# Kernel optimization log

Hardware: AMD Instinct MI355X
Metric: run time of the kernel (lower is better)

## Reference

```python
import jax, jax.numpy as jnp
import numpy as np

IMAGE_SIZE = 128
PATCH_SIZE = 8
BOND_DIM = 128
CP_RANK = 64
EMBED_DIM = 512
BATCH = 512
GRID = IMAGE_SIZE // PATCH_SIZE            # 16
NUM_PATCHES = GRID * GRID                  # 256
DEPTH = 4                                  # log4(256)
LEVEL_NODES = [64, 16, 4, 1]


def setup_inputs() -> dict:
    key = jax.random.key(0)
    ks = jax.random.split(key, 32)
    s = 0.02
    inp = {
        "x": jax.random.normal(ks[0], (BATCH, 1, IMAGE_SIZE, IMAGE_SIZE), jnp.float32),
        "W_patch": jax.random.normal(ks[1], (PATCH_SIZE * PATCH_SIZE, BOND_DIM), jnp.float32) * s,
        "b_patch": jnp.zeros((BOND_DIM,), jnp.float32),
        "pos": jax.random.normal(ks[2], (1, NUM_PATCHES, BOND_DIM), jnp.float32),
        "gamma": jnp.ones((BOND_DIM,), jnp.float32),
        "beta": jnp.zeros((BOND_DIM,), jnp.float32),
        "W_head": jax.random.normal(ks[3], (BOND_DIM, EMBED_DIM), jnp.float32) * s,
        "b_head": jnp.zeros((EMBED_DIM,), jnp.float32),
    }
    for lvl, n in enumerate(LEVEL_NODES):
        # per-node distinct CP factors: 4 children in_dim->rank, then rank->out_dim
        inp[f"f{lvl}"] = jax.random.normal(ks[4 + 2 * lvl], (n, 4, BOND_DIM, CP_RANK), jnp.float32) * s
        inp[f"o{lvl}"] = jax.random.normal(ks[5 + 2 * lvl], (n, CP_RANK, BOND_DIM), jnp.float32) * s
    return inp


def _patchify(x):
    # 'b c (h p1) (w p2) -> b (h w) (p1 p2 c)', c == 1
    b = x.shape[0]
    x = x.reshape(b, 1, GRID, PATCH_SIZE, GRID, PATCH_SIZE)
    x = x.transpose(0, 2, 4, 3, 5, 1)                  # b h w p1 p2 c
    return x.reshape(b, NUM_PATCHES, PATCH_SIZE * PATCH_SIZE)


def _quad_group(x, grid):
    # 'b (h w) c -> b (h/2 w/2) (h2 w2) c' with 2x2 blocks
    b, _, c = x.shape
    g2 = grid // 2
    x = x.reshape(b, g2, 2, g2, 2, c).transpose(0, 1, 3, 2, 4, 5)
    return x.reshape(b, g2 * g2, 4, c)


def _cp_level(x, f, o):
    # x: [b, n, 4, C]; f: [n, 4, C, R]; o: [n, R, C]
    u = jnp.einsum('bnqc,nqcr->bnqr', x, f)
    p = jnp.prod(u, axis=2)                            # [b, n, R]
    return jnp.einsum('bnr,nrc->bnc', p, o)


def reference(x, W_patch, b_patch, pos, f0, o0, f1, o1, f2, o2, f3, o3,
              gamma, beta, W_head, b_head):
    h = _patchify(x) @ W_patch + b_patch               # [b, 256, C]
    h = h + pos
    grid = GRID
    for f, o in ((f0, o0), (f1, o1), (f2, o2), (f3, o3)):
        h = _cp_level(_quad_group(h, grid), f, o)
        grid //= 2
    h = h[:, 0, :]                                     # squeeze node dim
    mu = jnp.mean(h, axis=-1, keepdims=True)
    var = jnp.var(h, axis=-1, keepdims=True)
    h = (h - mu) / jnp.sqrt(var + 1e-5) * gamma + beta
    out = h @ W_head + b_head
    n = jnp.maximum(jnp.linalg.norm(out, axis=-1, keepdims=True), 1e-12)
    return out / n
```

## Files before the change

### kernel.cpp

```cpp
#include <hip/hip_runtime.h>
#include <hip/hip_bf16.h>

#define BATCH     512
#define IMG       128
#define PS        8
#define GRID_P    16
#define NP        256
#define C         128
#define R         64
#define E         512

typedef float f32x4 __attribute__((ext_vector_type(4)));
typedef short s16x8 __attribute__((ext_vector_type(8)));

__device__ __forceinline__ unsigned short f2bf(float x) {
    unsigned int u = __float_as_uint(x);
    u += 0x7fffu + ((u >> 16) & 1u);
    return (unsigned short)(u >> 16);
}
__device__ __forceinline__ float bf2f(unsigned short h) {
    return __uint_as_float(((unsigned int)h) << 16);
}

__global__ __launch_bounds__(256) void prep_kernel(
    const float* __restrict__ f0, const float* __restrict__ f1,
    const float* __restrict__ f2, const float* __restrict__ f3,
    const float* __restrict__ o0, const float* __restrict__ o1,
    const float* __restrict__ o2, const float* __restrict__ o3,
    const float* __restrict__ Wh, const float* __restrict__ Wp,
    unsigned short* __restrict__ fT, unsigned short* __restrict__ oT,
    unsigned short* __restrict__ WhT, unsigned short* __restrict__ Wp_bf)
{
    __shared__ float ls[128 * 68];
    const int bi = blockIdx.x, t = threadIdx.x;

    if (bi < 340) {
        const float* src;
        if      (bi < 256) src = f0 + (size_t)bi * 8192;
        else if (bi < 320) src = f1 + (size_t)(bi - 256) * 8192;
        else if (bi < 336) src = f2 + (size_t)(bi - 320) * 8192;
        else               src = f3 + (size_t)(bi - 336) * 8192;
        unsigned short* dst = fT + (size_t)bi * 8192;
#pragma unroll
        for (int i = 0; i < 8; ++i) {
            const int fi = (t + 256 * i) * 4;
            const int c = fi >> 6, r = fi & 63;
            *(float4*)(ls + c * 68 + r) = *(const float4*)(src + fi);
        }
        __syncthreads();
        const int rr = t >> 2, seg = t & 3;
        unsigned int* d32 = (unsigned int*)(dst + rr * 128 + seg * 32);
#pragma unroll
        for (int ii = 0; ii < 16; ++ii) {
            const int c = seg * 32 + ii * 2;
            const unsigned int lo = f2bf(ls[c * 68 + rr]);
            const unsigned int hi = f2bf(ls[(c + 1) * 68 + rr]);
            d32[ii] = lo | (hi << 16);
        }
    } else if (bi < 425) {
        const int oi = bi - 340;
        const float* src;
        if      (oi < 64) src = o0 + (size_t)oi * 8192;
        else if (oi < 80) src = o1 + (size_t)(oi - 64) * 8192;
        else if (oi < 84) src = o2 + (size_t)(oi - 80) * 8192;
        else              src = o3 + (size_t)(oi - 84) * 8192;
        unsigned short* dst = oT + (size_t)oi * 8192;
#pragma unroll
        for (int i = 0; i < 8; ++i) {
            const int fi = (t + 256 * i) * 4;
            const int r = fi >> 7, c = fi & 127;
            *(float4*)(ls + r * 132 + c) = *(const float4*)(src + fi);
        }
        __syncthreads();
        const int cc = t >> 1, seg = t & 1;
        unsigned int* d32 = (unsigned int*)(dst + cc * 64 + seg * 32);
#pragma unroll
        for (int ii = 0; ii < 16; ++ii) {
            const int r = seg * 32 + ii * 2;
            const unsigned int lo = f2bf(ls[r * 132 + cc]);
            const unsigned int hi = f2bf(ls[(r + 1) * 132 + cc]);
            d32[ii] = lo | (hi << 16);
        }
    } else if (bi < 433) {
        const int j = bi - 425;
#pragma unroll
        for (int i = 0; i < 8; ++i) {
            const int fi = (t + 256 * i) * 4;
            const int c = fi >> 6, e = fi & 63;
            *(float4*)(ls + c * 68 + e) = *(const float4*)(Wh + (size_t)c * E + j * 64 + e);
        }
        __syncthreads();
        const int rr = t >> 2, seg = t & 3;
        unsigned int* d32 = (unsigned int*)(WhT + (size_t)(j * 64 + rr) * 128 + seg * 32);
#pragma unroll
        for (int ii = 0; ii < 16; ++ii) {
            const int c = seg * 32 + ii * 2;
            const unsigned int lo = f2bf(ls[c * 68 + rr]);
            const unsigned int hi = f2bf(ls[(c + 1) * 68 + rr]);
            d32[ii] = lo | (hi << 16);
        }
    } else {
#pragma unroll
        for (int i = 0; i < 32; ++i) {
            const int idx = i * 256 + t;
            Wp_bf[idx] = f2bf(Wp[idx]);
        }
    }
}

__global__ __launch_bounds__(64) void wft_pf_kernel(
    const unsigned short* __restrict__ fT0,
    const unsigned short* __restrict__ Wp_bf,
    const float* __restrict__ pos, const float* __restrict__ bp,
    unsigned short* __restrict__ WfT,
    float* __restrict__ pf)
{
    const int bi = blockIdx.x;
    if (bi < 256) {
        const int blk  = bi;
        const int lane = threadIdx.x & 63;
        const int m = lane & 15, g = lane >> 4;
        const unsigned short* A = fT0 + (size_t)blk * 8192;

        f32x4 acc[4][4];
#pragma unroll
        for (int mt = 0; mt < 4; ++mt)
#pragma unroll
            for (int nt = 0; nt < 4; ++nt) acc[mt][nt] = (f32x4){0.f, 0.f, 0.f, 0.f};

#pragma unroll
        for (int kt = 0; kt < 4; ++kt) {
            const int koff = kt * 32 + g * 8;
            s16x8 afr[4], bfr[4];
#pragma unroll
            for (int mt = 0; mt < 4; ++mt)
                afr[mt] = *(const s16x8*)(A + (size_t)(mt * 16 + m) * 128 + koff);
#pragma unroll
            for (int nt = 0; nt < 4; ++nt)
                bfr[nt] = *(const s16x8*)(Wp_bf + (size_t)(nt * 16 + m) * 128 + koff);
#pragma unroll
            for (int mt = 0; mt < 4; ++mt)
#pragma unroll
                for (int nt = 0; nt < 4; ++nt)
                    acc[mt][nt] = __builtin_amdgcn_mfma_f32_16x16x32_bf16(afr[mt], bfr[nt], acc[mt][nt], 0, 0, 0);
        }

        unsigned short* D = WfT + (size_t)blk * 4096;
#pragma unroll
        for (int mt = 0; mt < 4; ++mt)
#pragma unroll
            for (int nt = 0; nt < 4; ++nt)
#pragma unroll
                for (int j = 0; j < 4; ++j)
                    D[(size_t)(mt * 16 + g * 4 + j) * 64 + nt * 16 + m] = f2bf(acc[mt][nt][j]);
    } else {
        const int blk = bi - 256;
        const int n = blk >> 2, q = blk & 3;
        const int r = threadIdx.x & 63;
        const int p = (2 * (n >> 3) + (q >> 1)) * GRID_P + 2 * (n & 7) + (q & 1);
        const unsigned short* frow = fT0 + (size_t)blk * 8192 + (size_t)r * 128;
        const float* pp = pos + (size_t)p * C;
        float s = 0.f;
#pragma unroll 4
        for (int c = 0; c < C; ++c) s += (pp[c] + bp[c]) * bf2f(frow[c]);
        pf[blk * 64 + r] = s;
    }
}

__global__ __launch_bounds__(256) void cp_level0_fused(
    const float* __restrict__ x,
    const unsigned short* __restrict__ WfT,
    const float* __restrict__ pf,
    const unsigned short* __restrict__ oT0,
    unsigned short* __restrict__ h1)
{
    constexpr int NN = 64;
    __shared__ __align__(16) float us[4 * 16 * 68];
    __shared__ __align__(16) unsigned short ps[16 * 72];

    const int bi = blockIdx.x;
    const int n = bi >> 5, btile = bi & 31;
    const int t = threadIdx.x, w = t >> 6, lane = t & 63;
    const int m = lane & 15, g = lane >> 4;
    const int bt = btile * 16;
    const int y1 = n >> 3, x1 = n & 7;
    const int b = bt + m;
    const int q = w;

    const int py = (2 * y1 + (q >> 1)) * PS;
    const int px = (2 * x1 + (q & 1)) * PS;
    s16x8 a[2];
#pragma unroll
    for (int kt = 0; kt < 2; ++kt) {
        const float* src = x + ((size_t)b * IMG + py + kt * 4 + g) * IMG + px;
        const float4 p0 = *(const float4*)src;
        const float4 p1 = *(const float4*)(src + 4);
        s16x8 v;
        v[0] = (short)f2bf(p0.x); v[1] = (short)f2bf(p0.y);
        v[2] = (short)f2bf(p0.z); v[3] = (short)f2bf(p0.w);
        v[4] = (short)f2bf(p1.x); v[5] = (short)f2bf(p1.y);
        v[6] = (short)f2bf(p1.z); v[7] = (short)f2bf(p1.w);
        a[kt] = v;
    }

    const float* pfq = pf + (size_t)(n * 4 + q) * 64;
    f32x4 acc_u[4];
#pragma unroll
    for (int nt = 0; nt < 4; ++nt) {
        const float pv = pfq[nt * 16 + m];
        acc_u[nt] = (f32x4){pv, pv, pv, pv};
    }
    const unsigned short* Wq = WfT + (size_t)(n * 4 + q) * 4096;
#pragma unroll
    for (int kt = 0; kt < 2; ++kt) {
        const int koff = kt * 32 + g * 8;
#pragma unroll
        for (int nt = 0; nt < 4; ++nt) {
            const s16x8 bfr = *(const s16x8*)(Wq + (size_t)(nt * 16 + m) * 64 + koff);
            acc_u[nt] = __builtin_amdgcn_mfma_f32_16x16x32_bf16(a[kt], bfr, acc_u[nt], 0, 0, 0);
        }
    }
#pragma unroll
    for (int nt = 0; nt < 4; ++nt)
#pragma unroll
        for (int j = 0; j < 4; ++j)
            us[(q * 16 + g * 4 + j) * 68 + nt * 16 + m] = acc_u[nt][j];
    __syncthreads();

    {
        const int pb = t >> 4, r0 = (t & 15) * 4;
        const f32x4 u0 = *(const f32x4*)(us + (0 * 16 + pb) * 68 + r0);
        const f32x4 u1 = *(const f32x4*)(us + (1 * 16 + pb) * 68 + r0);
        const f32x4 u2 = *(const f32x4*)(us + (2 * 16 + pb) * 68 + r0);
        const f32x4 u3 = *(const f32x4*)(us + (3 * 16 + pb) * 68 + r0);
        const f32x4 p = u0 * u1 * u2 * u3;
        uint2 v;
        v.x = (unsigned int)f2bf(p[0]) | ((unsigned int)f2bf(p[1]) << 16);
        v.y = (unsigned int)f2bf(p[2]) | ((unsigned int)f2bf(p[3]) << 16);
        *(uint2*)(ps + pb * 72 + r0) = v;
    }
    __syncthreads();

    const unsigned short* oTn = oT0 + (size_t)n * C * R;
    s16x8 ap[2];
#pragma unroll
    for (int kt = 0; kt < 2; ++kt)
        ap[kt] = *(const s16x8*)(ps + m * 72 + kt * 32 + g * 8);
    f32x4 aco[2];
#pragma unroll
    for (int i = 0; i < 2; ++i) {
        aco[i] = (f32x4){0.f, 0.f, 0.f, 0.f};
        const int ct = w * 2 + i;
#pragma unroll
        for (int kt = 0; kt < 2; ++kt) {
            const s16x8 bfr = *(const s16x8*)(oTn + (size_t)(ct * 16 + m) * R + kt * 32 + g * 8);
            aco[i] = __builtin_amdgcn_mfma_f32_16x16x32_bf16(ap[kt], bfr, aco[i], 0, 0, 0);
        }
    }
#pragma unroll
    for (int i = 0; i < 2; ++i)
#pragma unroll
        for (int j = 0; j < 4; ++j) {
            const int row = bt + g * 4 + j;
            h1[((size_t)row * NN + n) * C + (w * 2 + i) * 16 + m] = f2bf(aco[i][j]);
        }
}

template<int NN, int GIN>
__global__ __launch_bounds__(256) void cp_level_mfma4(
    const unsigned short* __restrict__ hin,
    const unsigned short* __restrict__ fT,
    const unsigned short* __restrict__ oT,
    unsigned short* __restrict__ hout)
{
    constexpr int NIN = GIN * GIN;
    constexpr int G2  = GIN / 2;
    __shared__ __align__(16) float us[4 * 16 * 68];
    __shared__ __align__(16) unsigned short ps[16 * 72];

    const int bi = blockIdx.x;
    const int n = bi >> 5, btile = bi & 31;
    const int t = threadIdx.x, w = t >> 6, lane = t & 63;
    const int m = lane & 15, g = lane >> 4;
    const int bt = btile * 16;
    const int y1 = n / G2, x1 = n % G2;
    const int q = w;

    const int pidx = (2 * y1 + (q >> 1)) * GIN + 2 * x1 + (q & 1);
    const unsigned short* xq = hin + ((size_t)(bt + m) * NIN + pidx) * C;
    const unsigned short* fq = fT + (size_t)(n * 4 + q) * R * C;

    f32x4 acc_u[4];
#pragma unroll
    for (int nt = 0; nt < 4; ++nt) acc_u[nt] = (f32x4){0.f, 0.f, 0.f, 0.f};
#pragma unroll
    for (int kt = 0; kt < 4; ++kt) {
        const int koff = kt * 32 + g * 8;
        const s16x8 a = *(const s16x8*)(xq + koff);
#pragma unroll
        for (int nt = 0; nt < 4; ++nt) {
            const s16x8 bfr = *(const s16x8*)(fq + (size_t)(nt * 16 + m) * C + koff);
            acc_u[nt] = __builtin_amdgcn_mfma_f32_16x16x32_bf16(a, bfr, acc_u[nt], 0, 0, 0);
        }
    }
#pragma unroll
    for (int nt = 0; nt < 4; ++nt)
#pragma unroll
        for (int j = 0; j < 4; ++j)
            us[(q * 16 + g * 4 + j) * 68 + nt * 16 + m] = acc_u[nt][j];
    __syncthreads();

    {
        const int pb = t >> 4, r0 = (t & 15) * 4;
        const f32x4 u0 = *(const f32x4*)(us + (0 * 16 + pb) * 68 + r0);
        const f32x4 u1 = *(const f32x4*)(us + (1 * 16 + pb) * 68 + r0);
        const f32x4 u2 = *(const f32x4*)(us + (2 * 16 + pb) * 68 + r0);
        const f32x4 u3 = *(const f32x4*)(us + (3 * 16 + pb) * 68 + r0);
        const f32x4 p = u0 * u1 * u2 * u3;
        uint2 v;
        v.x = (unsigned int)f2bf(p[0]) | ((unsigned int)f2bf(p[1]) << 16);
        v.y = (unsigned int)f2bf(p[2]) | ((unsigned int)f2bf(p[3]) << 16);
        *(uint2*)(ps + pb * 72 + r0) = v;
    }
    __syncthreads();

    const unsigned short* oTn = oT + (size_t)n * C * R;
    s16x8 ap[2];
#pragma unroll
    for (int kt = 0; kt < 2; ++kt)
        ap[kt] = *(const s16x8*)(ps + m * 72 + kt * 32 + g * 8);
    f32x4 aco[2];
#pragma unroll
    for (int i = 0; i < 2; ++i) {
        aco[i] = (f32x4){0.f, 0.f, 0.f, 0.f};
        const int ct = w * 2 + i;
#pragma unroll
        for (int kt = 0; kt < 2; ++kt) {
            const s16x8 bfr = *(const s16x8*)(oTn + (size_t)(ct * 16 + m) * R + kt * 32 + g * 8);
            aco[i] = __builtin_amdgcn_mfma_f32_16x16x32_bf16(ap[kt], bfr, aco[i], 0, 0, 0);
        }
    }
#pragma unroll
    for (int i = 0; i < 2; ++i)
#pragma unroll
        for (int j = 0; j < 4; ++j) {
            const int row = bt + g * 4 + j;
            hout[((size_t)row * NN + n) * C + (w * 2 + i) * 16 + m] = f2bf(aco[i][j]);
        }
}

__global__ __launch_bounds__(256) void tail_kernel(
    const unsigned short* __restrict__ h2,
    const unsigned short* __restrict__ fT2,
    const unsigned short* __restrict__ oT2,
    const unsigned short* __restrict__ fT3,
    const unsigned short* __restrict__ oT3,
    const float* __restrict__ gamma, const float* __restrict__ beta,
    const unsigned short* __restrict__ WhT,
    const float* __restrict__ bh,
    float* __restrict__ out)
{
    __shared__ __align__(16) float          us3[4 * 16 * 68];
    __shared__ __align__(16) unsigned short ps2[4 * 16 * 72];
    __shared__ __align__(16) unsigned short ps3[16 * 72];
    __shared__ __align__(16) unsigned short h3s[16 * 4 * 136];
    __shared__ __align__(16) float          h4s[16 * 132];
    __shared__ __align__(16) unsigned short hns[16 * 136];
    __shared__ float red[16 * 4];

    const int bt = blockIdx.x * 16;
    const int t = threadIdx.x, w = t >> 6, lane = t & 63;
    const int m = lane & 15, g = lane >> 4;

    {
        const int n2 = w;
        const int y1 = n2 >> 1, x1 = n2 & 1;
        f32x4 acc_u[4][4];
#pragma unroll
        for (int q = 0; q < 4; ++q)
#pragma unroll
            for (int nt = 0; nt < 4; ++nt) acc_u[q][nt] = (f32x4){0.f, 0.f, 0.f, 0.f};
#pragma unroll
        for (int q = 0; q < 4; ++q) {
            const int pidx = (2 * y1 + (q >> 1)) * 4 + 2 * x1 + (q & 1);
            const unsigned short* xq = h2 + ((size_t)(bt + m) * 16 + pidx) * C;
            const unsigned short* fq = fT2 + (size_t)(n2 * 4 + q) * R * C;
#pragma unroll
            for (int kt = 0; kt < 4; ++kt) {
                const int koff = kt * 32 + g * 8;
                const s16x8 a = *(const s16x8*)(xq + koff);
#pragma unroll
                for (int nt = 0; nt < 4; ++nt) {
                    const s16x8 bfr = *(const s16x8*)(fq + (size_t)(nt * 16 + m) * C + koff);
                    acc_u[q][nt] = __builtin_amdgcn_mfma_f32_16x16x32_bf16(a, bfr, acc_u[q][nt], 0, 0, 0);
                }
            }
        }
        f32x4 p[4];
#pragma unroll
        for (int nt = 0; nt < 4; ++nt)
            p[nt] = acc_u[0][nt] * acc_u[1][nt] * acc_u[2][nt] * acc_u[3][nt];
        unsigned short* myps = ps2 + w * 16 * 72;
#pragma unroll
        for (int nt = 0; nt < 4; ++nt)
#pragma unroll
            for (int j = 0; j < 4; ++j)
                myps[(g * 4 + j) * 72 + nt * 16 + m] = f2bf(p[nt][j]);

        f32x4 aco[8];
#pragma unroll
        for (int ct = 0; ct < 8; ++ct) aco[ct] = (f32x4){0.f, 0.f, 0.f, 0.f};
        const unsigned short* oTn = oT2 + (size_t)n2 * C * R;
#pragma unroll
        for (int kt = 0; kt < 2; ++kt) {
            const int koff = kt * 32 + g * 8;
            const s16x8 a = *(const s16x8*)(myps + m * 72 + koff);
#pragma unroll
            for (int ct = 0; ct < 8; ++ct) {
                const s16x8 bfr = *(const s16x8*)(oTn + (size_t)(ct * 16 + m) * R + koff);
                aco[ct] = __builtin_amdgcn_mfma_f32_16x16x32_bf16(a, bfr, aco[ct], 0, 0, 0);
            }
        }
#pragma unroll
        for (int ct = 0; ct < 8; ++ct)
#pragma unroll
            for (int j = 0; j < 4; ++j)
                h3s[((g * 4 + j) * 4 + n2) * 136 + ct * 16 + m] = f2bf(aco[ct][j]);
    }
    __syncthreads();

    {
        const int q = w;
        const unsigned short* fq = fT3 + (size_t)q * R * C;
        f32x4 acc_u[4];
#pragma unroll
        for (int nt = 0; nt < 4; ++nt) acc_u[nt] = (f32x4){0.f, 0.f, 0.f, 0.f};
#pragma unroll
        for (int kt = 0; kt < 4; ++kt) {
            const int koff = kt * 32 + g * 8;
            const s16x8 a = *(const s16x8*)(h3s + (m * 4 + q) * 136 + koff);
#pragma unroll
            for (int nt = 0; nt < 4; ++nt) {
                const s16x8 bfr = *(const s16x8*)(fq + (size_t)(nt * 16 + m) * C + koff);
                acc_u[nt] = __builtin_amdgcn_mfma_f32_16x16x32_bf16(a, bfr, acc_u[nt], 0, 0, 0);
            }
        }
#pragma unroll
        for (int nt = 0; nt < 4; ++nt)
#pragma unroll
            for (int j = 0; j < 4; ++j)
                us3[(q * 16 + g * 4 + j) * 68 + nt * 16 + m] = acc_u[nt][j];
    }
    __syncthreads();
    {
        const int pb = t >> 4, r0 = (t & 15) * 4;
        const f32x4 u0 = *(const f32x4*)(us3 + (0 * 16 + pb) * 68 + r0);
        const f32x4 u1 = *(const f32x4*)(us3 + (1 * 16 + pb) * 68 + r0);
        const f32x4 u2 = *(const f32x4*)(us3 + (2 * 16 + pb) * 68 + r0);
        const f32x4 u3 = *(const f32x4*)(us3 + (3 * 16 + pb) * 68 + r0);
        const f32x4 p = u0 * u1 * u2 * u3;
        uint2 v;
        v.x = (unsigned int)f2bf(p[0]) | ((unsigned int)f2bf(p[1]) << 16);
        v.y = (unsigned int)f2bf(p[2]) | ((unsigned int)f2bf(p[3]) << 16);
        *(uint2*)(ps3 + pb * 72 + r0) = v;
    }
    __syncthreads();
    {
        s16x8 ap[2];
#pragma unroll
        for (int kt = 0; kt < 2; ++kt)
            ap[kt] = *(const s16x8*)(ps3 + m * 72 + kt * 32 + g * 8);
#pragma unroll
        for (int i = 0; i < 2; ++i) {
            f32x4 aco = (f32x4){0.f, 0.f, 0.f, 0.f};
            const int ct = w * 2 + i;
#pragma unroll
            for (int kt = 0; kt < 2; ++kt) {
                const s16x8 bfr = *(const s16x8*)(oT3 + (size_t)(ct * 16 + m) * R + kt * 32 + g * 8);
                aco = __builtin_amdgcn_mfma_f32_16x16x32_bf16(ap[kt], bfr, aco, 0, 0, 0);
            }
#pragma unroll
            for (int j = 0; j < 4; ++j)
                h4s[(g * 4 + j) * 132 + ct * 16 + m] = aco[j];
        }
    }
    __syncthreads();

    {
        const int rb = w * 4 + g;
        const int c0 = m * 8;
        const f32x4 v0 = *(const f32x4*)(h4s + rb * 132 + c0);
        const f32x4 v1 = *(const f32x4*)(h4s + rb * 132 + c0 + 4);
        float s  = v0[0] + v0[1] + v0[2] + v0[3] + v1[0] + v1[1] + v1[2] + v1[3];
        float ss = v0[0]*v0[0] + v0[1]*v0[1] + v0[2]*v0[2] + v0[3]*v0[3]
                 + v1[0]*v1[0] + v1[1]*v1[1] + v1[2]*v1[2] + v1[3]*v1[3];
#pragma unroll
        for (int off = 1; off < 16; off <<= 1) {
            s  += __shfl_xor(s, off);
            ss += __shfl_xor(ss, off);
        }
        const float mu   = s * (1.f / C);
        const float var  = ss * (1.f / C) - mu * mu;
        const float rstd = rsqrtf(var + 1e-5f);
        const f32x4 ga0 = *(const f32x4*)(gamma + c0);
        const f32x4 ga1 = *(const f32x4*)(gamma + c0 + 4);
        const f32x4 be0 = *(const f32x4*)(beta + c0);
        const f32x4 be1 = *(const f32x4*)(beta + c0 + 4);
        unsigned int o32[4];
        float hv[8];
#pragma unroll
        for (int k = 0; k < 4; ++k) hv[k]     = (v0[k] - mu) * rstd * ga0[k] + be0[k];
#pragma unroll
        for (int k = 0; k < 4; ++k) hv[4 + k] = (v1[k] - mu) * rstd * ga1[k] + be1[k];
#pragma unroll
        for (int k = 0; k < 4; ++k)
            o32[k] = (unsigned int)f2bf(hv[2*k]) | ((unsigned int)f2bf(hv[2*k+1]) << 16);
        *(uint4*)(hns + rb * 136 + c0) = *(uint4*)o32;
    }
    __syncthreads();

    {
        f32x4 acc[8];
#pragma unroll
        for (int nt = 0; nt < 8; ++nt) {
            const int e = w * 128 + nt * 16 + m;
            const float bv = bh[e];
            acc[nt] = (f32x4){bv, bv, bv, bv};
        }
#pragma unroll
        for (int kt = 0; kt < 4; ++kt) {
            const int koff = kt * 32 + g * 8;
            const s16x8 a = *(const s16x8*)(hns + m * 136 + koff);
#pragma unroll
            for (int nt = 0; nt < 8; ++nt) {
                const int e = w * 128 + nt * 16 + m;
                const s16x8 bfr = *(const s16x8*)(WhT + (size_t)e * 128 + koff);
                acc[nt] = __builtin_amdgcn_mfma_f32_16x16x32_bf16(a, bfr, acc[nt], 0, 0, 0);
            }
        }
        float sq[4];
#pragma unroll
        for (int j = 0; j < 4; ++j) {
            float s = 0.f;
#pragma unroll
            for (int nt = 0; nt < 8; ++nt) s += acc[nt][j] * acc[nt][j];
#pragma unroll
            for (int off = 1; off < 16; off <<= 1) s += __shfl_xor(s, off);
            sq[j] = s;
        }
        if (m == 0) {
#pragma unroll
            for (int j = 0; j < 4; ++j) red[(g * 4 + j) * 4 + w] = sq[j];
        }
        __syncthreads();
#pragma unroll
        for (int j = 0; j < 4; ++j) {
            const int row = g * 4 + j;
            const float tot = red[row * 4 + 0] + red[row * 4 + 1]
                            + red[row * 4 + 2] + red[row * 4 + 3];
            const float inv = 1.f / fmaxf(sqrtf(tot), 1e-12f);
#pragma unroll
            for (int nt = 0; nt < 8; ++nt) {
                const int e = w * 128 + nt * 16 + m;
                out[(size_t)(bt + row) * E + e] = acc[nt][j] * inv;
            }
        }
    }
}

extern "C" void kernel_launch(void* const* d_in, const int* in_sizes, int n_in,
                              void* d_out, int out_size, void* d_ws, size_t ws_size,
                              hipStream_t stream) {
    const float* x     = (const float*)d_in[0];
    const float* Wp    = (const float*)d_in[1];
    const float* bp    = (const float*)d_in[2];
    const float* pos   = (const float*)d_in[3];
    const float* gamma = (const float*)d_in[4];
    const float* beta  = (const float*)d_in[5];
    const float* Wh    = (const float*)d_in[6];
    const float* bh    = (const float*)d_in[7];
    const float* f0    = (const float*)d_in[8];
    const float* o0    = (const float*)d_in[9];
    const float* f1    = (const float*)d_in[10];
    const float* o1    = (const float*)d_in[11];
    const float* f2    = (const float*)d_in[12];
    const float* o2    = (const float*)d_in[13];
    const float* f3    = (const float*)d_in[14];
    const float* o3    = (const float*)d_in[15];
    float* out = (float*)d_out;

    unsigned short* h1  = (unsigned short*)d_ws;
    unsigned short* h2  = h1 + (size_t)4194304;
    unsigned short* fT  = h2 + (size_t)1048576;
    unsigned short* oT  = fT + (size_t)2785280;
    unsigned short* Wpb = oT + (size_t)696320;
    unsigned short* WfT = Wpb + (size_t)8192;
    unsigned short* WhT = WfT + (size_t)1048576;
    float*          pff = (float*)(WhT + 65536);

    unsigned short* fT0 = fT;
    unsigned short* fT1 = fT + (size_t)256 * 8192;
    unsigned short* fT2 = fT + (size_t)320 * 8192;
    unsigned short* fT3 = fT + (size_t)336 * 8192;
    unsigned short* oT0 = oT;
    unsigned short* oT1 = oT + (size_t)64 * 8192;
    unsigned short* oT2 = oT + (size_t)80 * 8192;
    unsigned short* oT3 = oT + (size_t)84 * 8192;

    prep_kernel<<<434, 256, 0, stream>>>(f0, f1, f2, f3, o0, o1, o2, o3,
                                         Wh, Wp, fT, oT, WhT, Wpb);
    wft_pf_kernel<<<512, 64, 0, stream>>>(fT0, Wpb, pos, bp, WfT, pff);

    cp_level0_fused<<<64 * 32, 256, 0, stream>>>(x, WfT, pff, oT0, h1);
    cp_level_mfma4<16, 8><<<16 * 32, 256, 0, stream>>>(h1, fT1, oT1, h2);
    tail_kernel<<<32, 256, 0, stream>>>(h2, fT2, oT2, fT3, oT3,
                                        gamma, beta, WhT, bh, out);
}
```

Measured before the change: 165.5 us.

## Fuse weight prep kernels and merge CP levels 0 and 1 into one kernel

Folds the patch-weight folding (WfT) and positional bias projection (pf) into the prep kernel, computing directly from fp32 f0 in shared memory. This drops the bf16 transposed copy of f0 and the separate wft_pf launch. Levels 0 and 1 of the tree are fused: each block handles one level-1 node, with each wave computing a full level-0 node and keeping h1 in shared memory. This removes the h1 global round trip and one launch, but gives a smaller grid (512 blocks instead of 2048) and more work per wave.

After: 156.5 us. -5.4%, faster.

```diff
diff --git a/kernel.cpp b/kernel.cpp
--- a/kernel.cpp
+++ b/kernel.cpp
@@ -22,25 +22,86 @@
     return __uint_as_float(((unsigned int)h) << 16);
 }
 
-__global__ __launch_bounds__(256) void prep_kernel(
+__global__ __launch_bounds__(256) void prep_all_kernel(
     const float* __restrict__ f0, const float* __restrict__ f1,
     const float* __restrict__ f2, const float* __restrict__ f3,
     const float* __restrict__ o0, const float* __restrict__ o1,
     const float* __restrict__ o2, const float* __restrict__ o3,
     const float* __restrict__ Wh, const float* __restrict__ Wp,
-    unsigned short* __restrict__ fT, unsigned short* __restrict__ oT,
-    unsigned short* __restrict__ WhT, unsigned short* __restrict__ Wp_bf)
+    const float* __restrict__ pos, const float* __restrict__ bp,
+    unsigned short* __restrict__ fTL, unsigned short* __restrict__ oT,
+    unsigned short* __restrict__ WhT, unsigned short* __restrict__ WfT,
+    float* __restrict__ pf)
 {
     __shared__ float ls[128 * 68];
+    __shared__ float red[64 * 4];
     const int bi = blockIdx.x, t = threadIdx.x;
 
-    if (bi < 340) {
+    if (bi < 256) {
+        const float* src = f0 + (size_t)bi * 8192;
+#pragma unroll
+        for (int i = 0; i < 8; ++i) {
+            const int fi = (t + 256 * i) * 4;
+            const int c = fi >> 6, r = fi & 63;
+            *(float4*)(ls + c * 68 + r) = *(const float4*)(src + fi);
+        }
+        __syncthreads();
+
+        const int w = t >> 6, lane = t & 63;
+        const int m = lane & 15, g = lane >> 4;
+
+        f32x4 acc[4];
+#pragma unroll
+        for (int nt = 0; nt < 4; ++nt) acc[nt] = (f32x4){0.f, 0.f, 0.f, 0.f};
+#pragma unroll
+        for (int kt = 0; kt < 4; ++kt) {
+            s16x8 afr;
+#pragma unroll
+            for (int e = 0; e < 8; ++e)
+                afr[e] = (short)f2bf(ls[(kt * 32 + g * 8 + e) * 68 + w * 16 + m]);
+#pragma unroll
+            for (int nt = 0; nt < 4; ++nt) {
+                const float* wr = Wp + (size_t)(nt * 16 + m) * 128 + kt * 32 + g * 8;
+                const float4 b0 = *(const float4*)wr;
+                const float4 b1 = *(const float4*)(wr + 4);
+                s16x8 bfr;
+                bfr[0] = (short)f2bf(b0.x); bfr[1] = (short)f2bf(b0.y);
+                bfr[2] = (short)f2bf(b0.z); bfr[3] = (short)f2bf(b0.w);
+                bfr[4] = (short)f2bf(b1.x); bfr[5] = (short)f2bf(b1.y);
+                bfr[6] = (short)f2bf(b1.z); bfr[7] = (short)f2bf(b1.w);
+                acc[nt] = __builtin_amdgcn_mfma_f32_16x16x32_bf16(afr, bfr, acc[nt], 0, 0, 0);
+            }
+        }
+        unsigned short* D = WfT + (size_t)bi * 4096;
+#pragma unroll
+        for (int nt = 0; nt < 4; ++nt)
+#pragma unroll
+            for (int j = 0; j < 4; ++j)
+                D[(size_t)(w * 16 + g * 4 + j) * 64 + nt * 16 + m] = f2bf(acc[nt][j]);
+
+        {
+            const int r = t & 63, half = t >> 6;
+            const int n0 = bi >> 2, q = bi & 3;
+            const int pp = (2 * (n0 >> 3) + (q >> 1)) * GRID_P + 2 * (n0 & 7) + (q & 1);
+            const float* posr = pos + (size_t)pp * C;
+            float s = 0.f;
+#pragma unroll 8
+            for (int e = 0; e < 32; ++e) {
+                const int c = half * 32 + e;
+                s += (posr[c] + bp[c]) * ls[c * 68 + r];
+            }
+            red[r * 4 + half] = s;
+        }
+        __syncthreads();
+        if (t < 64)
+            pf[bi * 64 + t] = red[t * 4 + 0] + red[t * 4 + 1] + red[t * 4 + 2] + red[t * 4 + 3];
+    } else if (bi < 340) {
+        const int ti = bi - 256;
         const float* src;
-        if      (bi < 256) src = f0 + (size_t)bi * 8192;
-        else if (bi < 320) src = f1 + (size_t)(bi - 256) * 8192;
-        else if (bi < 336) src = f2 + (size_t)(bi - 320) * 8192;
-        else               src = f3 + (size_t)(bi - 336) * 8192;
-        unsigned short* dst = fT + (size_t)bi * 8192;
+        if      (ti < 64) src = f1 + (size_t)ti * 8192;
+        else if (ti < 80) src = f2 + (size_t)(ti - 64) * 8192;
+        else              src = f3 + (size_t)(ti - 80) * 8192;
+        unsigned short* dst = fTL + (size_t)ti * 8192;
 #pragma unroll
         for (int i = 0; i < 8; ++i) {
             const int fi = (t + 256 * i) * 4;
@@ -81,7 +142,7 @@
             const unsigned int hi = f2bf(ls[(r + 1) * 132 + cc]);
             d32[ii] = lo | (hi << 16);
         }
-    } else if (bi < 433) {
+    } else {
         const int j = bi - 425;
 #pragma unroll
         for (int i = 0; i < 8; ++i) {
@@ -99,254 +160,163 @@
             const unsigned int hi = f2bf(ls[(c + 1) * 68 + rr]);
             d32[ii] = lo | (hi << 16);
         }
-    } else {
-#pragma unroll
-        for (int i = 0; i < 32; ++i) {
-            const int idx = i * 256 + t;
-            Wp_bf[idx] = f2bf(Wp[idx]);
-        }
     }
 }
 
-__global__ __launch_bounds__(64) void wft_pf_kernel(
-    const unsigned short* __restrict__ fT0,
-    const unsigned short* __restrict__ Wp_bf,
-    const float* __restrict__ pos, const float* __restrict__ bp,
-    unsigned short* __restrict__ WfT,
-    float* __restrict__ pf)
-{
-    const int bi = blockIdx.x;
-    if (bi < 256) {
-        const int blk  = bi;
-        const int lane = threadIdx.x & 63;
-        const int m = lane & 15, g = lane >> 4;
-        const unsigned short* A = fT0 + (size_t)blk * 8192;
-
-        f32x4 acc[4][4];
-#pragma unroll
-        for (int mt = 0; mt < 4; ++mt)
-#pragma unroll
-            for (int nt = 0; nt < 4; ++nt) acc[mt][nt] = (f32x4){0.f, 0.f, 0.f, 0.f};
-
-#pragma unroll
-        for (int kt = 0; kt < 4; ++kt) {
-            const int koff = kt * 32 + g * 8;
-            s16x8 afr[4], bfr[4];
-#pragma unroll
-            for (int mt = 0; mt < 4; ++mt)
-                afr[mt] = *(const s16x8*)(A + (size_t)(mt * 16 + m) * 128 + koff);
-#pragma unroll
-            for (int nt = 0; nt < 4; ++nt)
-                bfr[nt] = *(const s16x8*)(Wp_bf + (size_t)(nt * 16 + m) * 128 + koff);
-#pragma unroll
-            for (int mt = 0; mt < 4; ++mt)
-#pragma unroll
-                for (int nt = 0; nt < 4; ++nt)
-                    acc[mt][nt] = __builtin_amdgcn_mfma_f32_16x16x32_bf16(afr[mt], bfr[nt], acc[mt][nt], 0, 0, 0);
-        }
-
-        unsigned short* D = WfT + (size_t)blk * 4096;
-#pragma unroll
-        for (int mt = 0; mt < 4; ++mt)
-#pragma unroll
-            for (int nt = 0; nt < 4; ++nt)
-#pragma unroll
-                for (int j = 0; j < 4; ++j)
-                    D[(size_t)(mt * 16 + g * 4 + j) * 64 + nt * 16 + m] = f2bf(acc[mt][nt][j]);
-    } else {
-        const int blk = bi - 256;
-        const int n = blk >> 2, q = blk & 3;
-        const int r = threadIdx.x & 63;
-        const int p = (2 * (n >> 3) + (q >> 1)) * GRID_P + 2 * (n & 7) + (q & 1);
-        const unsigned short* frow = fT0 + (size_t)blk * 8192 + (size_t)r * 128;
-        const float* pp = pos + (size_t)p * C;
-        float s = 0.f;
-#pragma unroll 4
-        for (int c = 0; c < C; ++c) s += (pp[c] + bp[c]) * bf2f(frow[c]);
-        pf[blk * 64 + r] = s;
-    }
-}
-
-__global__ __launch_bounds__(256) void cp_level0_fused(
+__global__ __launch_bounds__(256) void level01_fused(
     const float* __restrict__ x,
     const unsigned short* __restrict__ WfT,
     const float* __restrict__ pf,
-    const unsigned short* __restrict__ oT0,
-    unsigned short* __restrict__ h1)
+    const unsigned short* __restrict__ oT,
+    const unsigned short* __restrict__ fT1,
+    unsigned short* __restrict__ h2)
 {
-    constexpr int NN = 64;
-    __shared__ __align__(16) float us[4 * 16 * 68];
-    __shared__ __align__(16) unsigned short ps[16 * 72];
+    __shared__ __align__(16) float          us1[4 * 16 * 68];
+    __shared__ __align__(16) unsigned short ps0[4 * 16 * 72];
+    __shared__ __align__(16) unsigned short ps1[16 * 72];
+    __shared__ __align__(16) unsigned short h1s[4 * 16 * 136];
 
     const int bi = blockIdx.x;
-    const int n = bi >> 5, btile = bi & 31;
+    const int n1 = bi >> 5, btile = bi & 31;
     const int t = threadIdx.x, w = t >> 6, lane = t & 63;
     const int m = lane & 15, g = lane >> 4;
     const int bt = btile * 16;
-    const int y1 = n >> 3, x1 = n & 7;
-    const int b = bt + m;
-    const int q = w;
-
-    const int py = (2 * y1 + (q >> 1)) * PS;
-    const int px = (2 * x1 + (q & 1)) * PS;
-    s16x8 a[2];
-#pragma unroll
-    for (int kt = 0; kt < 2; ++kt) {
-        const float* src = x + ((size_t)b * IMG + py + kt * 4 + g) * IMG + px;
-        const float4 p0 = *(const float4*)src;
-        const float4 p1 = *(const float4*)(src + 4);
-        s16x8 v;
-        v[0] = (short)f2bf(p0.x); v[1] = (short)f2bf(p0.y);
-        v[2] = (short)f2bf(p0.z); v[3] = (short)f2bf(p0.w);
-        v[4] = (short)f2bf(p1.x); v[5] = (short)f2bf(p1.y);
-        v[6] = (short)f2bf(p1.z); v[7] = (short)f2bf(p1.w);
-        a[kt] = v;
-    }
-
-    const float* pfq = pf + (size_t)(n * 4 + q) * 64;
-    f32x4 acc_u[4];
+    const int b  = bt + m;
+
+    const int n0 = (2 * (n1 >> 2) + (w >> 1)) * 8 + 2 * (n1 & 3) + (w & 1);
+    const int y0 = n0 >> 3, x0 = n0 & 7;
+
+    s16x8 a[4][2];
+#pragma unroll
+    for (int q = 0; q < 4; ++q) {
+        const int py = (2 * y0 + (q >> 1)) * PS;
+        const int px = (2 * x0 + (q & 1)) * PS;
+#pragma unroll
+        for (int kt = 0; kt < 2; ++kt) {
+            const float* src = x + ((size_t)b * IMG + py + kt * 4 + g) * IMG + px;
+            const float4 p0 = *(const float4*)src;
+            const float4 p1 = *(const float4*)(src + 4);
+            s16x8 v;
+            v[0] = (short)f2bf(p0.x); v[1] = (short)f2bf(p0.y);
+            v[2] = (short)f2bf(p0.z); v[3] = (short)f2bf(p0.w);
+            v[4] = (short)f2bf(p1.x); v[5] = (short)f2bf(p1.y);
+            v[6] = (short)f2bf(p1.z); v[7] = (short)f2bf(p1.w);
+            a[q][kt] = v;
+        }
+    }
+
+    f32x4 accu[4][4];
+#pragma unroll
+    for (int q = 0; q < 4; ++q) {
+        const float* pfq = pf + (size_t)(n0 * 4 + q) * 64;
+#pragma unroll
+        for (int nt = 0; nt < 4; ++nt) {
+            const float pv = pfq[nt * 16 + m];
+            accu[q][nt] = (f32x4){pv, pv, pv, pv};
+        }
+    }
+#pragma unroll
+    for (int q = 0; q < 4; ++q) {
+        const unsigned short* Wq = WfT + (size_t)(n0 * 4 + q) * 4096;
+#pragma unroll
+        for (int kt = 0; kt < 2; ++kt) {
+            const int koff = kt * 32 + g * 8;
+#pragma unroll
+            for (int nt = 0; nt < 4; ++nt) {
+                const s16x8 bfr = *(const s16x8*)(Wq + (size_t)(nt * 16 + m) * 64 + koff);
+                accu[q][nt] = __builtin_amdgcn_mfma_f32_16x16x32_bf16(a[q][kt], bfr, accu[q][nt], 0, 0, 0);
+            }
+        }
+    }
+
+    unsigned short* myps = ps0 + w * (16 * 72);
 #pragma unroll
     for (int nt = 0; nt < 4; ++nt) {
-        const float pv = pfq[nt * 16 + m];
-        acc_u[nt] = (f32x4){pv, pv, pv, pv};
-    }
-    const unsigned short* Wq = WfT + (size_t)(n * 4 + q) * 4096;
-#pragma unroll
-    for (int kt = 0; kt < 2; ++kt) {
-        const int koff = kt * 32 + g * 8;
-#pragma unroll
-        for (int nt = 0; nt < 4; ++nt) {
-            const s16x8 bfr = *(const s16x8*)(Wq + (size_t)(nt * 16 + m) * 64 + koff);
-            acc_u[nt] = __builtin_amdgcn_mfma_f32_16x16x32_bf16(a[kt], bfr, acc_u[nt], 0, 0, 0);
-        }
-    }
-#pragma unroll
-    for (int nt = 0; nt < 4; ++nt)
+        const f32x4 pr = accu[0][nt] * accu[1][nt] * accu[2][nt] * accu[3][nt];
 #pragma unroll
         for (int j = 0; j < 4; ++j)
-            us[(q * 16 + g * 4 + j) * 68 + nt * 16 + m] = acc_u[nt][j];
+            myps[(g * 4 + j) * 72 + nt * 16 + m] = f2bf(pr[j]);
+    }
+
+    {
+        s16x8 ap[2];
+#pragma unroll
+        for (int kt = 0; kt < 2; ++kt)
+            ap[kt] = *(const s16x8*)(myps + m * 72 + kt * 32 + g * 8);
+        const unsigned short* oTn = oT + (size_t)n0 * 8192;
+        unsigned short* myh = h1s + w * (16 * 136);
+#pragma unroll
+        for (int ct = 0; ct < 8; ++ct) {
+            f32x4 aco = (f32x4){0.f, 0.f, 0.f, 0.f};
+#pragma unroll
+            for (int kt = 0; kt < 2; ++kt) {
+                const s16x8 bfr = *(const s16x8*)(oTn + (size_t)(ct * 16 + m) * 64 + kt * 32 + g * 8);
+                aco = __builtin_amdgcn_mfma_f32_16x16x32_bf16(ap[kt], bfr, aco, 0, 0, 0);
+            }
+#pragma unroll
+            for (int j = 0; j < 4; ++j)
+                myh[(g * 4 + j) * 136 + ct * 16 + m] = f2bf(aco[j]);
+        }
+    }
+
+    {
+        const unsigned short* myh = h1s + w * (16 * 136);
+        const unsigned short* fq = fT1 + (size_t)(n1 * 4 + w) * 8192;
+        f32x4 au[4];
+#pragma unroll
+        for (int nt = 0; nt < 4; ++nt) au[nt] = (f32x4){0.f, 0.f, 0.f, 0.f};
+#pragma unroll
+        for (int kt = 0; kt < 4; ++kt) {
+            const int koff = kt * 32 + g * 8;
+            const s16x8 afr = *(const s16x8*)(myh + m * 136 + koff);
+#pragma unroll
+            for (int nt = 0; nt < 4; ++nt) {
+                const s16x8 bfr = *(const s16x8*)(fq + (size_t)(nt * 16 + m) * 128 + koff);
+                au[nt] = __builtin_amdgcn_mfma_f32_16x16x32_bf16(afr, bfr, au[nt], 0, 0, 0);
+            }
+        }
+#pragma unroll
+        for (int nt = 0; nt < 4; ++nt)
+#pragma unroll
+            for (int j = 0; j < 4; ++j)
+                us1[(w * 16 + g * 4 + j) * 68 + nt * 16 + m] = au[nt][j];
+    }
     __syncthreads();
 
     {
         const int pb = t >> 4, r0 = (t & 15) * 4;
-        const f32x4 u0 = *(const f32x4*)(us + (0 * 16 + pb) * 68 + r0);
-        const f32x4 u1 = *(const f32x4*)(us + (1 * 16 + pb) * 68 + r0);
-        const f32x4 u2 = *(const f32x4*)(us + (2 * 16 + pb) * 68 + r0);
-        const f32x4 u3 = *(const f32x4*)(us + (3 * 16 + pb) * 68 + r0);
+        const f32x4 u0 = *(const f32x4*)(us1 + (0 * 16 + pb) * 68 + r0);
+        const f32x4 u1 = *(const f32x4*)(us1 + (1 * 16 + pb) * 68 + r0);
+        const f32x4 u2 = *(const f32x4*)(us1 + (2 * 16 + pb) * 68 + r0);
+        const f32x4 u3 = *(const f32x4*)(us1 + (3 * 16 + pb) * 68 + r0);
         const f32x4 p = u0 * u1 * u2 * u3;
         uint2 v;
         v.x = (unsigned int)f2bf(p[0]) | ((unsigned int)f2bf(p[1]) << 16);
         v.y = (unsigned int)f2bf(p[2]) | ((unsigned int)f2bf(p[3]) << 16);
-        *(uint2*)(ps + pb * 72 + r0) = v;
-    }
-    __syncthreads();
-
-    const unsigned short* oTn = oT0 + (size_t)n * C * R;
-    s16x8 ap[2];
-#pragma unroll
-    for (int kt = 0; kt < 2; ++kt)
-        ap[kt] = *(const s16x8*)(ps + m * 72 + kt * 32 + g * 8);
-    f32x4 aco[2];
-#pragma unroll
-    for (int i = 0; i < 2; ++i) {
-        aco[i] = (f32x4){0.f, 0.f, 0.f, 0.f};
-        const int ct = w * 2 + i;
-#pragma unroll
-        for (int kt = 0; kt < 2; ++kt) {
-            const s16x8 bfr = *(const s16x8*)(oTn + (size_t)(ct * 16 + m) * R + kt * 32 + g * 8);
-            aco[i] = __builtin_amdgcn_mfma_f32_16x16x32_bf16(ap[kt], bfr, aco[i], 0, 0, 0);
-        }
-    }
-#pragma unroll
-    for (int i = 0; i < 2; ++i)
-#pragma unroll
-        for (int j = 0; j < 4; ++j) {
-            const int row = bt + g * 4 + j;
-            h1[((size_t)row * NN + n) * C + (w * 2 + i) * 16 + m] = f2bf(aco[i][j]);
-        }
-}
-
-template<int NN, int GIN>
-__global__ __launch_bounds__(256) void cp_level_mfma4(
-    const unsigned short* __restrict__ hin,
-    const unsigned short* __restrict__ fT,
-    const unsigned short* __restrict__ oT,
-    unsigned short* __restrict__ hout)
-{
-    constexpr int NIN = GIN * GIN;
-    constexpr int G2  = GIN / 2;
-    __shared__ __align__(16) float us[4 * 16 * 68];
-    __shared__ __align__(16) unsigned short ps[16 * 72];
-
-    const int bi = blockIdx.x;
-    const int n = bi >> 5, btile = bi & 31;
-    const int t = threadIdx.x, w = t >> 6, lane = t & 63;
-    const int m = lane & 15, g = lane >> 4;
-    const int bt = btile * 16;
-    const int y1 = n / G2, x1 = n % G2;
-    const int q = w;
-
-    const int pidx = (2 * y1 + (q >> 1)) * GIN + 2 * x1 + (q & 1);
-    const unsigned short* xq = hin + ((size_t)(bt + m) * NIN + pidx) * C;
-    const unsigned short* fq = fT + (size_t)(n * 4 + q) * R * C;
-
-    f32x4 acc_u[4];
-#pragma unroll
-    for (int nt = 0; nt < 4; ++nt) acc_u[nt] = (f32x4){0.f, 0.f, 0.f, 0.f};
-#pragma unroll
-    for (int kt = 0; kt < 4; ++kt) {
-        const int koff = kt * 32 + g * 8;
-        const s16x8 a = *(const s16x8*)(xq + koff);
-#pragma unroll
-        for (int nt = 0; nt < 4; ++nt) {
-            const s16x8 bfr = *(const s16x8*)(fq + (size_t)(nt * 16 + m) * C + koff);
-            acc_u[nt] = __builtin_amdgcn_mfma_f32_16x16x32_bf16(a, bfr, acc_u[nt], 0, 0, 0);
-        }
-    }
-#pragma unroll
-    for (int nt = 0; nt < 4; ++nt)
-#pragma unroll
-        for (int j = 0; j < 4; ++j)
-            us[(q * 16 + g * 4 + j) * 68 + nt * 16 + m] = acc_u[nt][j];
-    __syncthreads();
-
-    {
-        const int pb = t >> 4, r0 = (t & 15) * 4;
-        const f32x4 u0 = *(const f32x4*)(us + (0 * 16 + pb) * 68 + r0);
-        const f32x4 u1 = *(const f32x4*)(us + (1 * 16 + pb) * 68 + r0);
-        const f32x4 u2 = *(const f32x4*)(us + (2 * 16 + pb) * 68 + r0);
-        const f32x4 u3 = *(const f32x4*)(us + (3 * 16 + pb) * 68 + r0);
-        const f32x4 p = u0 * u1 * u2 * u3;
-        uint2 v;
-        v.x = (unsigned int)f2bf(p[0]) | ((unsigned int)f2bf(p[1]) << 16);
-        v.y = (unsigned int)f2bf(p[2]) | ((unsigned int)f2bf(p[3]) << 16);
-        *(uint2*)(ps + pb * 72 + r0) = v;
-    }
-    __syncthreads();
-
-    const unsigned short* oTn = oT + (size_t)n * C * R;
-    s16x8 ap[2];
-#pragma unroll
-    for (int kt = 0; kt < 2; ++kt)
-        ap[kt] = *(const s16x8*)(ps + m * 72 + kt * 32 + g * 8);
-    f32x4 aco[2];
-#pragma unroll
-    for (int i = 0; i < 2; ++i) {
-        aco[i] = (f32x4){0.f, 0.f, 0.f, 0.f};
-        const int ct = w * 2 + i;
-#pragma unroll
-        for (int kt = 0; kt < 2; ++kt) {
-            const s16x8 bfr = *(const s16x8*)(oTn + (size_t)(ct * 16 + m) * R + kt * 32 + g * 8);
-            aco[i] = __builtin_amdgcn_mfma_f32_16x16x32_bf16(ap[kt], bfr, aco[i], 0, 0, 0);
-        }
-    }
-#pragma unroll
-    for (int i = 0; i < 2; ++i)
-#pragma unroll
-        for (int j = 0; j < 4; ++j) {
-            const int row = bt + g * 4 + j;
-            hout[((size_t)row * NN + n) * C + (w * 2 + i) * 16 + m] = f2bf(aco[i][j]);
-        }
+        *(uint2*)(ps1 + pb * 72 + r0) = v;
+    }
+    __syncthreads();
+
+    {
+        s16x8 ap[2];
+#pragma unroll
+        for (int kt = 0; kt < 2; ++kt)
+            ap[kt] = *(const s16x8*)(ps1 + m * 72 + kt * 32 + g * 8);
+        const unsigned short* oTn = oT + (size_t)(64 + n1) * 8192;
+#pragma unroll
+        for (int i = 0; i < 2; ++i) {
+            const int ct = w * 2 + i;
+            f32x4 aco = (f32x4){0.f, 0.f, 0.f, 0.f};
+#pragma unroll
+            for (int kt = 0; kt < 2; ++kt) {
+                const s16x8 bfr = *(const s16x8*)(oTn + (size_t)(ct * 16 + m) * 64 + kt * 32 + g * 8);
+                aco = __builtin_amdgcn_mfma_f32_16x16x32_bf16(ap[kt], bfr, aco, 0, 0, 0);
+            }
+#pragma unroll
+            for (int j = 0; j < 4; ++j)
+                h2[((size_t)(bt + g * 4 + j) * 16 + n1) * C + ct * 16 + m] = f2bf(aco[j]);
+        }
+    }
 }
 
 __global__ __launch_bounds__(256) void tail_kernel(
@@ -396,17 +366,14 @@
                 }
             }
         }
-        f32x4 p[4];
-#pragma unroll
-        for (int nt = 0; nt < 4; ++nt)
-            p[nt] = acc_u[0][nt] * acc_u[1][nt] * acc_u[2][nt] * acc_u[3][nt];
         unsigned short* myps = ps2 + w * 16 * 72;
 #pragma unroll
-        for (int nt = 0; nt < 4; ++nt)
-#pragma unroll
-            for (int j = 0; j < 4; ++j)
-                myps[(g * 4 + j) * 72 + nt * 16 + m] = f2bf(p[nt][j]);
-
+        for (int nt = 0; nt < 4; ++nt) {
+            const f32x4 p = acc_u[0][nt] * acc_u[1][nt] * acc_u[2][nt] * acc_u[3][nt];
+#pragma unroll
+            for (int j = 0; j < 4; ++j)
+                myps[(g * 4 + j) * 72 + nt * 16 + m] = f2bf(p[j]);
+        }
         f32x4 aco[8];
 #pragma unroll
         for (int ct = 0; ct < 8; ++ct) aco[ct] = (f32x4){0.f, 0.f, 0.f, 0.f};
@@ -589,30 +556,25 @@
     const float* o3    = (const float*)d_in[15];
     float* out = (float*)d_out;
 
-    unsigned short* h1  = (unsigned short*)d_ws;
-    unsigned short* h2  = h1 + (size_t)4194304;
-    unsigned short* fT  = h2 + (size_t)1048576;
-    unsigned short* oT  = fT + (size_t)2785280;
-    unsigned short* Wpb = oT + (size_t)696320;
-    unsigned short* WfT = Wpb + (size_t)8192;
+    unsigned short* h2  = (unsigned short*)d_ws;
+    unsigned short* fTL = h2 + (size_t)1048576;
+    unsigned short* oT  = fTL + (size_t)688128;
+    unsigned short* WfT = oT + (size_t)696320;
     unsigned short* WhT = WfT + (size_t)1048576;
     float*          pff = (float*)(WhT + 65536);
 
-    unsigned short* fT0 = fT;
-    unsigned short* fT1 = fT + (size_t)256 * 8192;
-    unsigned short* fT2 = fT + (size_t)320 * 8192;
-    unsigned short* fT3 = fT + (size_t)336 * 8192;
-    unsigned short* oT0 = oT;
-    unsigned short* oT1 = oT + (size_t)64 * 8192;
+    unsigned short* fT1 = fTL;
+    unsigned short* fT2 = fTL + (size_t)64 * 8192;
+    unsigned short* fT3 = fTL + (size_t)80 * 8192;
     unsigned short* oT2 = oT + (size_t)80 * 8192;
     unsigned short* oT3 = oT + (size_t)84 * 8192;
 
-    prep_kernel<<<434, 256, 0, stream>>>(f0, f1, f2, f3, o0, o1, o2, o3,
-                                         Wh, Wp, fT, oT, WhT, Wpb);
-    wft_pf_kernel<<<512, 64, 0, stream>>>(fT0, Wpb, pos, bp, WfT, pff);
-
-    cp_level0_fused<<<64 * 32, 256, 0, stream>>>(x, WfT, pff, oT0, h1);
-    cp_level_mfma4<16, 8><<<16 * 32, 256, 0, stream>>>(h1, fT1, oT1, h2);
+    prep_all_kernel<<<433, 256, 0, stream>>>(f0, f1, f2, f3, o0, o1, o2, o3,
+                                             Wh, Wp, pos, bp,
+                                             fTL, oT, WhT, WfT, pff);
+
+    level01_fused<<<16 * 32, 256, 0, stream>>>(x, WfT, pff, oT, fT1, h2);
+
     tail_kernel<<<32, 256, 0, stream>>>(h2, fT2, oT2, fT3, oT3,
                                         gamma, beta, WhT, bh, out);
 }
```
